# Optimization experiments

Measured on AMD Instinct MI355X. Metric: run time of the kernel, lower is better.

## Reference

```python
import jax, jax.numpy as jnp
import numpy as np

# Static config matching init_kwargs / input_specs
B, CIN, H, W = 4, 64, 128, 128
COUT, K, DG = 64, 3, 8
STRIDE, PAD, DIL = 1, 1, 1
HO = (H + 2 * PAD - DIL * (K - 1) - 1) // STRIDE + 1
WO = (W + 2 * PAD - DIL * (K - 1) - 1) // STRIDE + 1
KK = K * K
CG = CIN // DG  # channels per deformable group


def setup_inputs() -> dict:
    key = jax.random.key(0)
    k1, k2, k3, k4 = jax.random.split(key, 4)
    x = jax.random.normal(k1, (B, CIN, H, W), jnp.float32)
    offset = jax.random.normal(k2, (B, 2 * DG * KK, HO, WO), jnp.float32)
    s = 1.0 / np.sqrt(CIN * KK)  # matches reset_parameters stdv / fan_in bound
    weight = jax.random.uniform(k3, (COUT, CIN, K, K), jnp.float32, -s, s)
    bias = jax.random.uniform(k4, (COUT,), jnp.float32, -s, s)
    return {"x": x, "offset": offset, "weight": weight, "bias": bias}


def _deform_conv(x, offset, weight, bias):
    # offset layout (DCNv1): [B, DG * KK * 2, Ho, Wo], per kernel point (dy, dx)
    off = offset.reshape(B, DG, KK, 2, HO, WO)
    khs = (jnp.repeat(jnp.arange(K), K) * DIL).astype(jnp.float32)  # [KK] kernel dy
    kws = (jnp.tile(jnp.arange(K), K) * DIL).astype(jnp.float32)    # [KK] kernel dx
    gy = (jnp.arange(HO) * STRIDE - PAD).astype(jnp.float32)        # [Ho] base y
    gx = (jnp.arange(WO) * STRIDE - PAD).astype(jnp.float32)        # [Wo] base x
    # sampling positions: [B, DG, KK, Ho, Wo]
    py = gy[None, None, None, :, None] + khs[None, None, :, None, None] + off[:, :, :, 0]
    px = gx[None, None, None, None, :] + kws[None, None, :, None, None] + off[:, :, :, 1]
    y0 = jnp.floor(py)
    x0 = jnp.floor(px)
    ly = py - y0  # fractional parts
    lx = px - x0
    xg = x.reshape(B, DG, CG, H * W)  # channels grouped by deformable group

    def corner(yc, xc, wgt):
        # zero-padded bilinear: out-of-bounds corners contribute 0
        valid = (yc >= 0) & (yc < H) & (xc >= 0) & (xc < W)
        idx = (jnp.clip(yc, 0, H - 1) * W + jnp.clip(xc, 0, W - 1)).astype(jnp.int32)
        v = jnp.take_along_axis(xg, idx.reshape(B, DG, 1, KK * HO * WO), axis=3)
        v = v.reshape(B, DG, CG, KK, HO, WO)
        w = jnp.where(valid, wgt, 0.0)  # [B, DG, KK, Ho, Wo]
        return v * w[:, :, None]

    cols = (corner(y0, x0, (1.0 - ly) * (1.0 - lx))
            + corner(y0, x0 + 1.0, (1.0 - ly) * lx)
            + corner(y0 + 1.0, x0, ly * (1.0 - lx))
            + corner(y0 + 1.0, x0 + 1.0, ly * lx))  # [B, DG, CG, KK, Ho, Wo]

    wk = weight.reshape(COUT, DG, CG, KK)  # groups == 1
    out = jnp.einsum('bgcpyx,ogcp->boyx', cols, wk)
    return out + bias[None, :, None, None]


def reference(x, offset, weight, bias):
    return _deform_conv(x, offset, weight, bias)
```

## Files before the change

kernel.cpp:

```cpp
#include <hip/hip_runtime.h>

#define BB    4
#define CINT  64
#define HH    128
#define WW    128
#define COUT  64
#define DGN   8
#define CG    8
#define KKN   9
#define HO    128
#define WO    128
#define HOWO  16384
#define HWSZ  (HH * WW)
#define NKT   18

typedef __bf16 bf16x8 __attribute__((ext_vector_type(8)));
typedef float  f32x4  __attribute__((ext_vector_type(4)));

static __device__ __forceinline__ ushort f2bf(float f) {
    unsigned u = __builtin_bit_cast(unsigned, f);
    u += 0x7fffu + ((u >> 16) & 1u);
    return (ushort)(u >> 16);
}
static __device__ __forceinline__ float bf2f(ushort u) {
    return __builtin_bit_cast(float, (unsigned)u << 16);
}

__global__ void prep_w(const float* __restrict__ wgt, uint4* __restrict__ wout) {
    int i = blockIdx.x * 256 + threadIdx.x;
    if (i >= NKT * 4 * 64) return;
    int lane = i & 63;
    int mt   = (i >> 6) & 3;
    int kt   = i >> 8;
    int m = lane & 15, quad = lane >> 4;
    int o = mt * 16 + m;
    union { ushort u[8]; uint4 v; } pk;
#pragma unroll
    for (int j = 0; j < 8; ++j) {
        int k   = kt * 32 + quad * 8 + j;
        int gkk = k >> 3, c = k & 7;
        int g   = gkk / 9, kk = gkk - 9 * g;
        pk.u[j] = f2bf(wgt[(o * CINT + g * CG + c) * KKN + kk]);
    }
    wout[i] = pk.v;
}

__global__ void prep_x(const float* __restrict__ x, uint4* __restrict__ xh) {
    int i  = blockIdx.x * 256 + threadIdx.x;
    int yx = i & (HWSZ - 1);
    int bg = i >> 14;
    const float* xp = x + (size_t)bg * CG * HWSZ + yx;
    union { ushort u[8]; uint4 v; } pk;
#pragma unroll
    for (int c = 0; c < CG; ++c) pk.u[c] = f2bf(xp[c * HWSZ]);
    xh[i] = pk.v;
}

__global__ __launch_bounds__(256, 4) void dcn_mfma(
    const uint4* __restrict__ xh, const float* __restrict__ off,
    const uint4* __restrict__ wq, const float* __restrict__ bias,
    float* __restrict__ out)
{
    const int tid  = threadIdx.x;
    const int wave = tid >> 6;
    const int lane = tid & 63;
    const int n    = lane & 15;
    const int quad = lane >> 4;

    const int bid  = blockIdx.x;
    const int tile = ((bid & 7) << 7) | (bid >> 3);
    const int pix_base = tile * 64 + wave * 16;
    const int b        = pix_base >> 14;
    const int rem_base = pix_base & 16383;
    const int rem      = rem_base + n;
    const int ho = rem >> 7, wo = rem & 127;
    const float fy0 = (float)(ho - 1);
    const float fx0 = (float)(wo - 1);

    f32x4 acc[4];
#pragma unroll
    for (int mt = 0; mt < 4; ++mt) acc[mt] = (f32x4){0.f, 0.f, 0.f, 0.f};

    const uint4* xb = xh + (size_t)b * DGN * HWSZ;

#pragma unroll
    for (int kt = 0; kt < NKT; ++kt) {
        uint4 aw0 = wq[(kt * 4 + 0) * 64 + lane];
        uint4 aw1 = wq[(kt * 4 + 1) * 64 + lane];
        uint4 aw2 = wq[(kt * 4 + 2) * 64 + lane];
        uint4 aw3 = wq[(kt * 4 + 3) * 64 + lane];

        int gkk = kt * 4 + quad;
        int g = gkk / 9, kk = gkk - 9 * g;
        const float* offp = off + ((size_t)((b * DGN + g) * KKN + kk) * 2) * HOWO + rem;
        float dy = offp[0];
        float dx = offp[HOWO];
        float py  = fy0 + (float)(kk / 3) + dy;
        float pxx = fx0 + (float)(kk - (kk / 3) * 3) + dx;
        float y0f = floorf(py), x0f = floorf(pxx);
        int y0 = (int)y0f, x0 = (int)x0f;
        float ly = py - y0f, lx = pxx - x0f;
        float hy = 1.f - ly, hx = 1.f - lx;
        float w00 = hy * hx, w01 = hy * lx, w10 = ly * hx, w11 = ly * lx;
        int y1 = y0 + 1, x1 = x0 + 1;
        bool vy0 = (unsigned)y0 < (unsigned)HH, vy1 = (unsigned)y1 < (unsigned)HH;
        bool vx0 = (unsigned)x0 < (unsigned)WW, vx1 = (unsigned)x1 < (unsigned)WW;
        if (!(vy0 && vx0)) w00 = 0.f;
        if (!(vy0 && vx1)) w01 = 0.f;
        if (!(vy1 && vx0)) w10 = 0.f;
        if (!(vy1 && vx1)) w11 = 0.f;
        int y0c = min(max(y0, 0), HH - 1), y1c = min(max(y1, 0), HH - 1);
        int x0c = min(max(x0, 0), WW - 1), x1c = min(max(x1, 0), WW - 1);
        const uint4* xgp = xb + (size_t)g * HWSZ;
        uint4 q00 = xgp[y0c * WW + x0c];
        uint4 q01 = xgp[y0c * WW + x1c];
        uint4 q10 = xgp[y1c * WW + x0c];
        uint4 q11 = xgp[y1c * WW + x1c];
        const ushort* u00 = (const ushort*)&q00;
        const ushort* u01 = (const ushort*)&q01;
        const ushort* u10 = (const ushort*)&q10;
        const ushort* u11 = (const ushort*)&q11;
        union { ushort u[8]; bf16x8 v; } pk;
#pragma unroll
        for (int c = 0; c < CG; ++c) {
            float v = w00 * bf2f(u00[c]) + w01 * bf2f(u01[c])
                    + w10 * bf2f(u10[c]) + w11 * bf2f(u11[c]);
            pk.u[c] = f2bf(v);
        }
        bf16x8 bfrag = pk.v;

        acc[0] = __builtin_amdgcn_mfma_f32_16x16x32_bf16(
                     __builtin_bit_cast(bf16x8, aw0), bfrag, acc[0], 0, 0, 0);
        acc[1] = __builtin_amdgcn_mfma_f32_16x16x32_bf16(
                     __builtin_bit_cast(bf16x8, aw1), bfrag, acc[1], 0, 0, 0);
        acc[2] = __builtin_amdgcn_mfma_f32_16x16x32_bf16(
                     __builtin_bit_cast(bf16x8, aw2), bfrag, acc[2], 0, 0, 0);
        acc[3] = __builtin_amdgcn_mfma_f32_16x16x32_bf16(
                     __builtin_bit_cast(bf16x8, aw3), bfrag, acc[3], 0, 0, 0);
    }

    float* outp = out + (size_t)b * COUT * HOWO + rem_base + n;
#pragma unroll
    for (int mt = 0; mt < 4; ++mt) {
        const float4 bq = *(const float4*)&bias[mt * 16 + quad * 4];
#pragma unroll
        for (int r = 0; r < 4; ++r) {
            int o = mt * 16 + quad * 4 + r;
            outp[(size_t)o * HOWO] = acc[mt][r] + ((const float*)&bq)[r];
        }
    }
}

extern "C" void kernel_launch(void* const* d_in, const int* in_sizes, int n_in,
                              void* d_out, int out_size, void* d_ws, size_t ws_size,
                              hipStream_t stream) {
    const float* x    = (const float*)d_in[0];
    const float* off  = (const float*)d_in[1];
    const float* wgt  = (const float*)d_in[2];
    const float* bias = (const float*)d_in[3];
    float* out = (float*)d_out;

    uint4* xh = (uint4*)d_ws;
    uint4* wq = (uint4*)((char*)d_ws + 8388608);

    prep_x<<<dim3(BB * DGN * HWSZ / 256), dim3(256), 0, stream>>>(x, xh);
    prep_w<<<dim3(NKT), dim3(256), 0, stream>>>(wgt, wq);
    dcn_mfma<<<dim3(BB * HO * WO / 64), dim3(256), 0, stream>>>(xh, off, wq, bias, out);
}
```

Measured before the change: 123.0 us.

## Process two 16-pixel tiles per wave to reuse weight fragments across MFMAs

Each wave now covers 32 output pixels (two 16-wide halves of a row) instead of 16, so each block handles a full 128-pixel row and the grid is halved. Every weight fragment load from global memory now feeds eight MFMAs instead of four, cutting weight traffic per pixel. The bf16 packing also switches from round-to-nearest to plain truncation of the upper 16 bits, which saves ALU work but changes numerics slightly. Launch bounds drop to 3 blocks per SIMD to allow the extra accumulator and fragment registers, which may reduce occupancy and latency hiding for the gather loads.

```diff
diff --git a/kernel.cpp b/kernel.cpp
--- a/kernel.cpp
+++ b/kernel.cpp
@@ -56,7 +56,7 @@
     xh[i] = pk.v;
 }
 
-__global__ __launch_bounds__(256, 4) void dcn_mfma(
+__global__ __launch_bounds__(256, 3) void dcn_mfma(
     const uint4* __restrict__ xh, const float* __restrict__ off,
     const uint4* __restrict__ wq, const float* __restrict__ bias,
     float* __restrict__ out)
@@ -68,18 +68,22 @@
     const int quad = lane >> 4;
 
     const int bid  = blockIdx.x;
-    const int tile = ((bid & 7) << 7) | (bid >> 3);
-    const int pix_base = tile * 64 + wave * 16;
-    const int b        = pix_base >> 14;
-    const int rem_base = pix_base & 16383;
-    const int rem      = rem_base + n;
-    const int ho = rem >> 7, wo = rem & 127;
+    const int tile = ((bid & 7) << 6) | (bid >> 3);
+    const int pix_blk  = tile * 128;
+    const int b        = pix_blk >> 14;
+    const int rem_blk  = pix_blk & 16383;
+    const int ho       = rem_blk >> 7;
+    const int wo0      = wave * 32 + n;
+    const int rem0     = rem_blk + wo0;
     const float fy0 = (float)(ho - 1);
-    const float fx0 = (float)(wo - 1);
+    const float fx0 = (float)(wo0 - 1);
 
-    f32x4 acc[4];
+    f32x4 acc[4][2];
 #pragma unroll
-    for (int mt = 0; mt < 4; ++mt) acc[mt] = (f32x4){0.f, 0.f, 0.f, 0.f};
+    for (int mt = 0; mt < 4; ++mt) {
+        acc[mt][0] = (f32x4){0.f, 0.f, 0.f, 0.f};
+        acc[mt][1] = (f32x4){0.f, 0.f, 0.f, 0.f};
+    }
 
     const uint4* xb = xh + (size_t)b * DGN * HWSZ;
 
@@ -90,63 +94,77 @@
         uint4 aw2 = wq[(kt * 4 + 2) * 64 + lane];
         uint4 aw3 = wq[(kt * 4 + 3) * 64 + lane];
 
-        int gkk = kt * 4 + quad;
-        int g = gkk / 9, kk = gkk - 9 * g;
-        const float* offp = off + ((size_t)((b * DGN + g) * KKN + kk) * 2) * HOWO + rem;
-        float dy = offp[0];
-        float dx = offp[HOWO];
-        float py  = fy0 + (float)(kk / 3) + dy;
-        float pxx = fx0 + (float)(kk - (kk / 3) * 3) + dx;
-        float y0f = floorf(py), x0f = floorf(pxx);
-        int y0 = (int)y0f, x0 = (int)x0f;
-        float ly = py - y0f, lx = pxx - x0f;
-        float hy = 1.f - ly, hx = 1.f - lx;
-        float w00 = hy * hx, w01 = hy * lx, w10 = ly * hx, w11 = ly * lx;
-        int y1 = y0 + 1, x1 = x0 + 1;
-        bool vy0 = (unsigned)y0 < (unsigned)HH, vy1 = (unsigned)y1 < (unsigned)HH;
-        bool vx0 = (unsigned)x0 < (unsigned)WW, vx1 = (unsigned)x1 < (unsigned)WW;
-        if (!(vy0 && vx0)) w00 = 0.f;
-        if (!(vy0 && vx1)) w01 = 0.f;
-        if (!(vy1 && vx0)) w10 = 0.f;
-        if (!(vy1 && vx1)) w11 = 0.f;
-        int y0c = min(max(y0, 0), HH - 1), y1c = min(max(y1, 0), HH - 1);
-        int x0c = min(max(x0, 0), WW - 1), x1c = min(max(x1, 0), WW - 1);
+        const int gkk = kt * 4 + quad;
+        const int g = gkk / 9, kk = gkk - 9 * g;
+        const float kdy = (float)(kk / 3);
+        const float kdx = (float)(kk - (kk / 3) * 3);
+        const float* offb = off + ((size_t)((b * DGN + g) * KKN + kk) * 2) * HOWO + rem0;
         const uint4* xgp = xb + (size_t)g * HWSZ;
-        uint4 q00 = xgp[y0c * WW + x0c];
-        uint4 q01 = xgp[y0c * WW + x1c];
-        uint4 q10 = xgp[y1c * WW + x0c];
-        uint4 q11 = xgp[y1c * WW + x1c];
-        const ushort* u00 = (const ushort*)&q00;
-        const ushort* u01 = (const ushort*)&q01;
-        const ushort* u10 = (const ushort*)&q10;
-        const ushort* u11 = (const ushort*)&q11;
-        union { ushort u[8]; bf16x8 v; } pk;
+
+        bf16x8 bfrag[2];
 #pragma unroll
-        for (int c = 0; c < CG; ++c) {
-            float v = w00 * bf2f(u00[c]) + w01 * bf2f(u01[c])
-                    + w10 * bf2f(u10[c]) + w11 * bf2f(u11[c]);
-            pk.u[c] = f2bf(v);
+        for (int h = 0; h < 2; ++h) {
+            float dy = offb[h * 16];
+            float dx = offb[HOWO + h * 16];
+            float py  = fy0 + kdy + dy;
+            float pxx = fx0 + (float)(h * 16) + kdx + dx;
+            float y0f = floorf(py), x0f = floorf(pxx);
+            int y0 = (int)y0f, x0 = (int)x0f;
+            float ly = py - y0f, lx = pxx - x0f;
+            float hy = 1.f - ly, hx = 1.f - lx;
+            float w00 = hy * hx, w01 = hy * lx, w10 = ly * hx, w11 = ly * lx;
+            int y1 = y0 + 1, x1 = x0 + 1;
+            bool vy0 = (unsigned)y0 < (unsigned)HH, vy1 = (unsigned)y1 < (unsigned)HH;
+            bool vx0 = (unsigned)x0 < (unsigned)WW, vx1 = (unsigned)x1 < (unsigned)WW;
+            if (!(vy0 && vx0)) w00 = 0.f;
+            if (!(vy0 && vx1)) w01 = 0.f;
+            if (!(vy1 && vx0)) w10 = 0.f;
+            if (!(vy1 && vx1)) w11 = 0.f;
+            int y0c = min(max(y0, 0), HH - 1), y1c = min(max(y1, 0), HH - 1);
+            int x0c = min(max(x0, 0), WW - 1), x1c = min(max(x1, 0), WW - 1);
+            uint4 q00 = xgp[y0c * WW + x0c];
+            uint4 q01 = xgp[y0c * WW + x1c];
+            uint4 q10 = xgp[y1c * WW + x0c];
+            uint4 q11 = xgp[y1c * WW + x1c];
+            const ushort* u00 = (const ushort*)&q00;
+            const ushort* u01 = (const ushort*)&q01;
+            const ushort* u10 = (const ushort*)&q10;
+            const ushort* u11 = (const ushort*)&q11;
+            union { unsigned w[4]; bf16x8 v; } pk;
+#pragma unroll
+            for (int j = 0; j < 4; ++j) {
+                float v0 = w00 * bf2f(u00[2*j])   + w01 * bf2f(u01[2*j])
+                         + w10 * bf2f(u10[2*j])   + w11 * bf2f(u11[2*j]);
+                float v1 = w00 * bf2f(u00[2*j+1]) + w01 * bf2f(u01[2*j+1])
+                         + w10 * bf2f(u10[2*j+1]) + w11 * bf2f(u11[2*j+1]);
+                pk.w[j] = (__builtin_bit_cast(unsigned, v1) & 0xffff0000u)
+                        | (__builtin_bit_cast(unsigned, v0) >> 16);
+            }
+            bfrag[h] = pk.v;
         }
-        bf16x8 bfrag = pk.v;
 
-        acc[0] = __builtin_amdgcn_mfma_f32_16x16x32_bf16(
-                     __builtin_bit_cast(bf16x8, aw0), bfrag, acc[0], 0, 0, 0);
-        acc[1] = __builtin_amdgcn_mfma_f32_16x16x32_bf16(
-                     __builtin_bit_cast(bf16x8, aw1), bfrag, acc[1], 0, 0, 0);
-        acc[2] = __builtin_amdgcn_mfma_f32_16x16x32_bf16(
-                     __builtin_bit_cast(bf16x8, aw2), bfrag, acc[2], 0, 0, 0);
-        acc[3] = __builtin_amdgcn_mfma_f32_16x16x32_bf16(
-                     __builtin_bit_cast(bf16x8, aw3), bfrag, acc[3], 0, 0, 0);
+#pragma unroll
+        for (int h = 0; h < 2; ++h) {
+            acc[0][h] = __builtin_amdgcn_mfma_f32_16x16x32_bf16(
+                            __builtin_bit_cast(bf16x8, aw0), bfrag[h], acc[0][h], 0, 0, 0);
+            acc[1][h] = __builtin_amdgcn_mfma_f32_16x16x32_bf16(
+                            __builtin_bit_cast(bf16x8, aw1), bfrag[h], acc[1][h], 0, 0, 0);
+            acc[2][h] = __builtin_amdgcn_mfma_f32_16x16x32_bf16(
+                            __builtin_bit_cast(bf16x8, aw2), bfrag[h], acc[2][h], 0, 0, 0);
+            acc[3][h] = __builtin_amdgcn_mfma_f32_16x16x32_bf16(
+                            __builtin_bit_cast(bf16x8, aw3), bfrag[h], acc[3][h], 0, 0, 0);
+        }
     }
 
-    float* outp = out + (size_t)b * COUT * HOWO + rem_base + n;
+    float* outp = out + (size_t)b * COUT * HOWO + rem_blk + wave * 32 + n;
 #pragma unroll
     for (int mt = 0; mt < 4; ++mt) {
         const float4 bq = *(const float4*)&bias[mt * 16 + quad * 4];
 #pragma unroll
         for (int r = 0; r < 4; ++r) {
             int o = mt * 16 + quad * 4 + r;
-            outp[(size_t)o * HOWO] = acc[mt][r] + ((const float*)&bq)[r];
+            outp[(size_t)o * HOWO]      = acc[mt][0][r] + ((const float*)&bq)[r];
+            outp[(size_t)o * HOWO + 16] = acc[mt][1][r] + ((const float*)&bq)[r];
         }
     }
 }
@@ -165,5 +183,5 @@
 
     prep_x<<<dim3(BB * DGN * HWSZ / 256), dim3(256), 0, stream>>>(x, xh);
     prep_w<<<dim3(NKT), dim3(256), 0, stream>>>(wgt, wq);
-    dcn_mfma<<<dim3(BB * HO * WO / 64), dim3(256), 0, stream>>>(xh, off, wq, bias, out);
+    dcn_mfma<<<dim3(BB * HO * WO / 128), dim3(256), 0, stream>>>(xh, off, wq, bias, out);
 }
```

After: 126.0 us. 1.02x slower.
